# Kernel optimization log

Measured on AMD Instinct MI355X. Metric: run time of the kernel, lower is better.

The kernel has to match this reference:

```python
import jax, jax.numpy as jnp
import numpy as np
from jax import lax

S, B, D = 512, 64, 120          # seq_len, batch, input_dim
OC, K = 16, 6                   # conv out_channels, kernel_size
H, O = 1024, 48                 # lstm hidden, output_dim
AFTER_CONV = (D - K) + 1        # 115 (stride=1, pad=0, dil=1)
AFTER_POOL = AFTER_CONV - 1     # 114 (maxpool k=2, stride=1)
LSTM_IN = AFTER_POOL * OC       # 1824


def setup_inputs() -> dict:
    key = jax.random.key(0)
    ks = jax.random.split(key, 12)
    inp = {
        "input_": jax.random.normal(ks[0], (S, B, D), dtype=jnp.float32),
        "hidden": jnp.zeros((1, B, H), dtype=jnp.float32),
        "cell": jnp.zeros((1, B, H), dtype=jnp.float32),
        "conv_w": jax.random.normal(ks[1], (OC, 1, K), dtype=jnp.float32) * 0.1,
        "conv_b": jax.random.normal(ks[2], (OC,), dtype=jnp.float32) * 0.1,
        "w_ih": jax.random.normal(ks[3], (4 * H, LSTM_IN), dtype=jnp.float32) * 0.02,
        "w_hh": jax.random.normal(ks[4], (4 * H, H), dtype=jnp.float32) * 0.02,
        "b_ih": jax.random.normal(ks[5], (4 * H,), dtype=jnp.float32) * 0.02,
        "b_hh": jax.random.normal(ks[6], (4 * H,), dtype=jnp.float32) * 0.02,
        "h2h_w": jax.random.normal(ks[7], (H, H), dtype=jnp.float32) * 0.02,
        "h2h_b": jax.random.normal(ks[8], (H,), dtype=jnp.float32) * 0.02,
        "out_w": jax.random.normal(ks[9], (O, H), dtype=jnp.float32) * 0.02,
        "out_b": jax.random.normal(ks[10], (O,), dtype=jnp.float32) * 0.02,
    }
    return inp


def _forward(input_, hidden, cell, conv_w, conv_b, w_ih, w_hh, b_ih, b_hh,
             h2h_w, h2h_b, out_w, out_b):
    s, b, d = input_.shape
    # in_channels=1 -> context_len=0: per-step conv == batched conv over [S*B, 1, D]
    x = input_.reshape(s * b, 1, d)
    c = lax.conv_general_dilated(x, conv_w, window_strides=(1,), padding="VALID",
                                 dimension_numbers=("NCH", "OIH", "NCH"))
    c = jax.nn.relu(c + conv_b[None, :, None])            # [S*B, OC, AFTER_CONV]
    p = jnp.maximum(c[:, :, :-1], c[:, :, 1:])            # maxpool k=2 stride=1
    feat = p.reshape(s, b, -1)                            # [S, B, OC*AFTER_POOL]

    def step(carry, x_t):
        h, cst = carry
        gates = x_t @ w_ih.T + b_ih + h @ w_hh.T + b_hh   # [B, 4H]
        i, f, g, o = jnp.split(gates, 4, axis=-1)          # torch gate order i,f,g,o
        i = jax.nn.sigmoid(i); f = jax.nn.sigmoid(f)
        g = jnp.tanh(g); o = jax.nn.sigmoid(o)
        cst = f * cst + i * g
        h = o * jnp.tanh(cst)
        return (h, cst), h

    (_, _), hs = lax.scan(step, (hidden[0], cell[0]), feat)  # hs: [S, B, H]
    hs = jax.nn.relu(hs)
    h2 = jax.nn.relu(hs @ h2h_w.T + h2h_b)                # [S, B, H]
    logits = h2 @ out_w.T + out_b                         # [S, B, O]
    return jax.nn.log_softmax(logits, axis=-1)


def reference(input_, hidden, cell, conv_w, conv_b, w_ih, w_hh, b_ih, b_hh,
              h2h_w, h2h_b, out_w, out_b):
    return _forward(input_, hidden, cell, conv_w, conv_b, w_ih, w_hh, b_ih, b_hh,
                    h2h_w, h2h_b, out_w, out_b)
```

## Files before the change

### kernel.cpp

```cpp
#include <hip/hip_runtime.h>
#include <stdint.h>
#include <stddef.h>

#define kS 512
#define kB 64
#define kD 120
#define kOC 16
#define kKSZ 6
#define kPOOL 114
#define kLIN 1824
#define kLINP 1920
#define kH 1024
#define kG 4096
#define kO 48
#define kROWS (kS * kB)
#define RNB 256
#define SLOT 16384

typedef __attribute__((ext_vector_type(8))) short bf16x8;
typedef __attribute__((ext_vector_type(4))) float f32x4;

__device__ __forceinline__ unsigned short f32_to_bf16(float f) {
  unsigned u = __float_as_uint(f);
  u += 0x7FFFu + ((u >> 16) & 1u);
  return (unsigned short)(u >> 16);
}
__device__ __forceinline__ float bf16_to_f32(unsigned short h) {
  return __uint_as_float(((unsigned)h) << 16);
}
__device__ __forceinline__ float sigmoid_(float x) { return 1.f / (1.f + __expf(-x)); }
__device__ __forceinline__ float tanh_(float x) { return 1.f - 2.f / (__expf(2.f * x) + 1.f); }

__device__ __forceinline__ void load_lds_16(const void* g, void* l) {
  __builtin_amdgcn_global_load_lds((__attribute__((address_space(1))) void*)g,
                                   (__attribute__((address_space(3))) void*)l, 16, 0, 0);
}

__device__ __forceinline__ void bar_lgkm() {
  __builtin_amdgcn_sched_barrier(0);
  asm volatile("s_waitcnt lgkmcnt(0)" ::: "memory");
  __builtin_amdgcn_s_barrier();
  __builtin_amdgcn_sched_barrier(0);
}

__device__ __forceinline__ unsigned long long coh_load(const unsigned long long* p) {
  return __hip_atomic_load(p, __ATOMIC_RELAXED, __HIP_MEMORY_SCOPE_AGENT);
}
__device__ __forceinline__ void coh_store(unsigned long long* p, unsigned long long v) {
  __hip_atomic_store(p, v, __ATOMIC_RELAXED, __HIP_MEMORY_SCOPE_AGENT);
}
__device__ __forceinline__ int inval(unsigned long long q) {
  return ((q >> 7) & 0xFFull) == 0xFEull;
}

__global__ void convert_weights(const float* __restrict__ wih, const float* __restrict__ whh,
                                const float* __restrict__ h2hw, const float* __restrict__ outw,
                                const float* __restrict__ bih, const float* __restrict__ bhh,
                                unsigned short* __restrict__ wihb, unsigned short* __restrict__ whhb,
                                unsigned short* __restrict__ h2hwb, unsigned short* __restrict__ outwb,
                                float* __restrict__ bsum) {
  const size_t N0 = (size_t)kG * kLINP;
  const size_t N1 = (size_t)kG * kH;
  const size_t N2 = (size_t)kH * kH;
  const size_t N3 = (size_t)kO * kH;
  const size_t N4 = kG;
  const size_t TOT = N0 + N1 + N2 + N3 + N4;
  for (size_t i = (size_t)blockIdx.x * blockDim.x + threadIdx.x; i < TOT;
       i += (size_t)gridDim.x * blockDim.x) {
    if (i < N0) {
      const size_t row = i / kLINP;
      const int col = (int)(i % kLINP);
      wihb[i] = (col < kLIN) ? f32_to_bf16(wih[row * kLIN + col]) : 0;
    } else if (i < N0 + N1) whhb[i - N0] = f32_to_bf16(whh[i - N0]);
    else if (i < N0 + N1 + N2) h2hwb[i - N0 - N1] = f32_to_bf16(h2hw[i - N0 - N1]);
    else if (i < N0 + N1 + N2 + N3) outwb[i - N0 - N1 - N2] = f32_to_bf16(outw[i - N0 - N1 - N2]);
    else { size_t j = i - N0 - N1 - N2 - N3; bsum[j] = bih[j] + bhh[j]; }
  }
}

__global__ __launch_bounds__(256) void conv_pool(const float* __restrict__ x,
                                                 const float* __restrict__ cw,
                                                 const float* __restrict__ cb,
                                                 unsigned short* __restrict__ feat,
                                                 long row_base) {
  __shared__ float xs[8][kD];
  __shared__ float ws[kOC][kKSZ];
  __shared__ float bs[kOC];
  const int tid = threadIdx.x;
  const long grow0 = row_base + (long)blockIdx.x * 8;
  const long lrow0 = (long)blockIdx.x * 8;
  if (tid < kOC * kKSZ) ws[tid / kKSZ][tid % kKSZ] = cw[tid];
  if (tid < kOC) bs[tid] = cb[tid];
  for (int i = tid; i < 8 * kD; i += 256) xs[i / kD][i % kD] = x[grow0 * kD + i];
  __syncthreads();
  for (int r = 0; r < 8; ++r) {
    for (int idx = tid; idx < kLIN; idx += 256) {
      const int oc = idx / kPOOL, p = idx % kPOOL;
      float c0 = bs[oc], c1 = bs[oc];
#pragma unroll
      for (int k = 0; k < kKSZ; ++k) {
        c0 += xs[r][p + k] * ws[oc][k];
        c1 += xs[r][p + 1 + k] * ws[oc][k];
      }
      float v = fmaxf(fmaxf(c0, c1), 0.f);
      feat[(lrow0 + r) * kLINP + idx] = f32_to_bf16(v);
    }
    for (int idx = kLIN + tid; idx < kLINP; idx += 256)
      feat[(lrow0 + r) * kLINP + idx] = 0;
  }
}

__global__ __launch_bounds__(256) void gemm_bt_bf16(const unsigned short* __restrict__ A,
                                                    const unsigned short* __restrict__ B,
                                                    const float* __restrict__ bias,
                                                    unsigned short* __restrict__ C,
                                                    int N, int K) {
  __shared__ unsigned short Al[2][128 * 32];
  __shared__ unsigned short Bl[2][128 * 32];
  const int tid = threadIdx.x;
  const int lane = tid & 63;
  const int wid = tid >> 6;
  const int wm = wid >> 1, wn = wid & 1;
  const long bm = (long)blockIdx.x * 128;
  const long bn = (long)blockIdx.y * 128;
  const int NT = K / 32;

  f32x4 acc[4][4] = {};

  auto stage = [&](int buf, int kt) {
    const long k0 = (long)kt * 32;
#pragma unroll
    for (int rnd = 0; rnd < 2; ++rnd) {
      const int chunk = rnd * 256 + tid;
      const int r = chunk >> 2, c = chunk & 3;
      load_lds_16(A + (bm + r) * K + k0 + c * 8, &Al[buf][chunk * 8]);
      load_lds_16(B + (bn + r) * K + k0 + c * 8, &Bl[buf][chunk * 8]);
    }
  };

  stage(0, 0);
  __syncthreads();
  int buf = 0;
  for (int kt = 0; kt < NT; ++kt) {
    if (kt + 1 < NT) stage(buf ^ 1, kt + 1);
    bf16x8 af[4], bfr[4];
#pragma unroll
    for (int i = 0; i < 4; ++i) {
      const int ar = wm * 64 + i * 16 + (lane & 15);
      af[i] = *(const bf16x8*)&Al[buf][ar * 32 + (lane >> 4) * 8];
      const int bc = wn * 64 + i * 16 + (lane & 15);
      bfr[i] = *(const bf16x8*)&Bl[buf][bc * 32 + (lane >> 4) * 8];
    }
#pragma unroll
    for (int i = 0; i < 4; ++i)
#pragma unroll
      for (int j = 0; j < 4; ++j)
        acc[i][j] = __builtin_amdgcn_mfma_f32_16x16x32_bf16(af[i], bfr[j], acc[i][j], 0, 0, 0);
    __syncthreads();
    buf ^= 1;
  }

#pragma unroll
  for (int i = 0; i < 4; ++i) {
#pragma unroll
    for (int j = 0; j < 4; ++j) {
      const long col = bn + wn * 64 + j * 16 + (lane & 15);
      const float bv = bias[col];
#pragma unroll
      for (int e = 0; e < 4; ++e) {
        const long row = bm + wm * 64 + i * 16 + (lane >> 4) * 4 + e;
        C[row * N + col] = f32_to_bf16(fmaxf(acc[i][j][e] + bv, 0.f));
      }
    }
  }
}

__global__ __launch_bounds__(512, 2) void gemm256_m2(const unsigned short* __restrict__ A,
                                                     const unsigned short* __restrict__ B,
                                                     const float* __restrict__ bias,
                                                     unsigned short* __restrict__ C,
                                                     int Kp) {
  __shared__ unsigned short AL[2][2][128 * 64];
  __shared__ unsigned short BL[2][2][128 * 64];
  const int tid = threadIdx.x;
  const int lane = tid & 63;
  const int wid = tid >> 6;
  const int wm = wid >> 2;
  const int wn = wid & 3;
  const long bm = (long)blockIdx.x * 256;
  const long bn = (long)blockIdx.y * 256;
  const int iters = Kp / 128;
  const int nkt = iters * 2;

  f32x4 acc[8][4] = {};

  auto stageu = [&](int db, int op, int hf, int kt) {
    const unsigned short* S = op ? B : A;
    const long base = op ? bn : bm;
    unsigned short* L = op ? &BL[db][hf][0] : &AL[db][hf][0];
#pragma unroll
    for (int c = 0; c < 2; ++c) {
      const int ch = c * 512 + tid;
      const int r = ch >> 3;
      const int cb = (ch & 7) * 8;
      load_lds_16(S + (base + hf * 128 + r) * Kp + (long)kt * 64 + cb, L + r * 64 + cb);
    }
  };

#pragma unroll
  for (int kt = 0; kt < 2; ++kt)
#pragma unroll
    for (int u = 0; u < 4; ++u) stageu(0, u >> 1, u & 1, kt);
  __builtin_amdgcn_sched_barrier(0);
  asm volatile("s_waitcnt vmcnt(0)" ::: "memory");
  __builtin_amdgcn_s_barrier();
  __builtin_amdgcn_sched_barrier(0);

  int d = 0;
  for (int it = 0; it < iters; ++it, d ^= 1) {
    bf16x8 bfr[8];
#pragma unroll
    for (int p = 0; p < 8; ++p) {
      const int q = p & 3;
      const int kbase = (p >> 2) ? 1 : 0;
      if (q == 0) {
#pragma unroll
        for (int nf = 0; nf < 4; ++nf)
#pragma unroll
          for (int ks = 0; ks < 2; ++ks)
            bfr[nf * 2 + ks] = *(const bf16x8*)&BL[d][wn >> 1]
                [((wn & 1) * 64 + nf * 16 + (lane & 15)) * 64 + ks * 32 + (lane >> 4) * 8];
      }
      bf16x8 afr[2][2];
#pragma unroll
      for (int m2 = 0; m2 < 2; ++m2)
#pragma unroll
        for (int ks = 0; ks < 2; ++ks)
          afr[m2][ks] = *(const bf16x8*)&AL[d][wm]
              [((q * 2 + m2) * 16 + (lane & 15)) * 64 + ks * 32 + (lane >> 4) * 8];
      (void)kbase;
      const int ktN = it * 2 + 2 + (p >> 2);
      if (ktN < nkt) stageu(d ^ 1, q >> 1, q & 1, ktN);
      if (p == 3 || p == 7) {
        __builtin_amdgcn_sched_barrier(0);
        asm volatile("s_waitcnt vmcnt(8)" ::: "memory");
      }
      __builtin_amdgcn_s_barrier();
      __builtin_amdgcn_s_setprio(1);
#pragma unroll
      for (int m2 = 0; m2 < 2; ++m2)
#pragma unroll
        for (int nf = 0; nf < 4; ++nf)
#pragma unroll
          for (int ks = 0; ks < 2; ++ks)
            acc[q * 2 + m2][nf] = __builtin_amdgcn_mfma_f32_16x16x32_bf16(
                afr[m2][ks], bfr[nf * 2 + ks], acc[q * 2 + m2][nf], 0, 0, 0);
      __builtin_amdgcn_s_setprio(0);
      __builtin_amdgcn_s_barrier();
    }
  }


#pragma unroll
  for (int mf = 0; mf < 8; ++mf) {
#pragma unroll
    for (int nf = 0; nf < 4; ++nf) {
      const long col = bn + wn * 64 + nf * 16 + (lane & 15);
      const float bv = bias[col];
      const int g = (int)(col >> 10), ub = (int)((col >> 4) & 63), ur = (int)(col & 15);
#pragma unroll
      for (int e = 0; e < 4; ++e) {
        const long row = bm + wm * 128 + mf * 16 + (lane >> 4) * 4 + e;
        C[(row * 64 + ub) * 64 + g * 16 + ur] = f32_to_bf16(acc[mf][nf][e] + bv);
      }
    }
  }
}

__global__ __launch_bounds__(512) void lstm_rec(const unsigned short* __restrict__ xw,
                                                const unsigned short* __restrict__ whh,
                                                const float* __restrict__ h0,
                                                const float* __restrict__ c0,
                                                float* __restrict__ cst,
                                                unsigned long long* __restrict__ hbuf,
                                                unsigned short* __restrict__ hs,
                                                int nsteps, int first, int t0step) {
  __shared__ unsigned short Bl[64 * 1024];
  __shared__ unsigned short hstage[256];
  __shared__ unsigned pacc_h[8][2][4][64];
  const int tid = threadIdx.x;
  const int lane = tid & 63;
  const int kq = tid >> 6;
  const int urow = lane & 15;
  const int bq = lane >> 4;
  const int bid = blockIdx.x;
  const int ublk = bid & 63;
  const int bqtr = bid >> 6;
  const int u0 = ublk * 16;
  const bool gatewave = (kq < 4);
  const int gbL = bq * 4 + kq;
  const int gbW = bqtr * 16 + gbL;

  for (int idx = tid; idx < 64 * 128; idx += 512) {
    const int col = idx & 63;
    const int kc = idx >> 6;
    const int gcol = (col >> 4) * kH + u0 + (col & 15);
    *(bf16x8*)&Bl[kc * 512 + col * 8] = *(const bf16x8*)&whh[(long)gcol * kH + kc * 8];
  }
  float creg = 0.f;
  if (first) {
    if (tid < 64) {
      const int lb = tid >> 2, un4 = (tid & 3) * 4, gb = bqtr * 16 + lb;
      unsigned long long v = 0;
#pragma unroll
      for (int e = 0; e < 4; ++e) {
        const unsigned long long b16 = f32_to_bf16(h0[gb * kH + u0 + un4 + e]);
        v |= b16 << (16 * e);
      }
      coh_store(&hbuf[(size_t)ublk * 256 + gb * 4 + (tid & 3)], v);
    }
    if (gatewave) creg = c0[gbW * kH + u0 + urow];
  } else {
    if (gatewave) creg = cst[gbW * kH + u0 + urow];
  }
  bar_lgkm();

  float xv[4];
  auto load_xv = [&](int t) {
    const unsigned short* xp = xw + ((long)(t * kB + gbW) * 64 + ublk) * 64 + urow;
#pragma unroll
    for (int g = 0; g < 4; ++g) xv[g] = bf16_to_f32(xp[g * 16]);
  };
  if (gatewave) load_xv(0);

  const int ach = (bqtr * 16 + urow) * 4 + (bq & 1) * 2;

  for (int t = 0; t < nsteps; ++t) {
    const unsigned long long* curs = hbuf + (size_t)(t0step + t) * SLOT;
    unsigned long long* nxts = hbuf + (size_t)(t0step + t + 1) * SLOT;

    unsigned long long q[8];
#pragma unroll
    for (int i = 0; i < 8; ++i)
      q[i] = coh_load(curs + (size_t)((kq * 4 + (i >> 1)) * 2 + (bq >> 1)) * 256 + ach + (i & 1));
    for (;;) {
      int bad = 0;
#pragma unroll
      for (int i = 0; i < 8; ++i) bad |= inval(q[i]);
      if (!bad) break;
      unsigned long long t2[8];
#pragma unroll
      for (int i = 0; i < 8; ++i)
        t2[i] =
            coh_load(curs + (size_t)((kq * 4 + (i >> 1)) * 2 + (bq >> 1)) * 256 + ach + (i & 1));
#pragma unroll
      for (int i = 0; i < 8; ++i) q[i] = t2[i];
    }

    f32x4 acc[4] = {};
#pragma unroll
    for (int ktl = 0; ktl < 4; ++ktl) {
      union { unsigned long long qq[2]; bf16x8 v; } a;
      a.qq[0] = q[2 * ktl];
      a.qq[1] = q[2 * ktl + 1];
      const int kc = (kq * 4 + ktl) * 4 + bq;
#pragma unroll
      for (int g = 0; g < 4; ++g) {
        const bf16x8 bb = *(const bf16x8*)&Bl[kc * 512 + (g * 16 + urow) * 8];
        acc[g] = __builtin_amdgcn_mfma_f32_16x16x32_bf16(a.v, bb, acc[g], 0, 0, 0);
      }
    }

#pragma unroll
    for (int j = 0; j < 4; ++j)
#pragma unroll
      for (int gp = 0; gp < 2; ++gp) {
        const unsigned lo = f32_to_bf16(acc[2 * gp][j]);
        const unsigned hi = f32_to_bf16(acc[2 * gp + 1][j]);
        pacc_h[kq][gp][j][lane] = lo | (hi << 16);
      }
    bar_lgkm();

    if (gatewave) {
      float s[4] = {xv[0], xv[1], xv[2], xv[3]};
#pragma unroll
      for (int p = 0; p < 8; ++p) {
        const unsigned v0 = pacc_h[p][0][kq][lane];
        const unsigned v1 = pacc_h[p][1][kq][lane];
        s[0] += bf16_to_f32((unsigned short)v0);
        s[1] += bf16_to_f32((unsigned short)(v0 >> 16));
        s[2] += bf16_to_f32((unsigned short)v1);
        s[3] += bf16_to_f32((unsigned short)(v1 >> 16));
      }
      const float gi = sigmoid_(s[0]);
      const float gf = sigmoid_(s[1]);
      const float gg = tanh_(s[2]);
      const float go = sigmoid_(s[3]);
      creg = gf * creg + gi * gg;
      hstage[gbL * 16 + urow] = f32_to_bf16(go * tanh_(creg));
      asm volatile("" ::: "memory");
      if (lane < 16) {
        const int lb = (lane >> 2) * 4 + kq;
        const int e = lane & 3;
        unsigned long long qp = 0;
#pragma unroll
        for (int x = 0; x < 4; ++x)
          qp |= ((unsigned long long)hstage[lb * 16 + e * 4 + x]) << (16 * x);
        coh_store(&nxts[(size_t)ublk * 256 + (bqtr * 16 + lb) * 4 + e], qp);
        unsigned long long r = 0;
#pragma unroll
        for (int x = 0; x < 4; ++x) {
          unsigned long long sv = (qp >> (16 * x)) & 0xFFFFull;
          if (sv & 0x8000ull) sv = 0;
          r |= sv << (16 * x);
        }
        *(unsigned long long*)&hs[(long)(t * kB + bqtr * 16 + lb) * kH + u0 + e * 4] = r;
      }
      if (t + 1 < nsteps) load_xv(t + 1);
    }
    bar_lgkm();
  }

  if (gatewave) cst[gbW * kH + u0 + urow] = creg;
}

__global__ __launch_bounds__(256) void out_head(const unsigned short* __restrict__ h2,
                                                const unsigned short* __restrict__ ow,
                                                const float* __restrict__ ob,
                                                float* __restrict__ out) {
  __shared__ unsigned short Wl[48 * 1024];
  const int tid = threadIdx.x;
  const int lane = tid & 63;
  const int w = tid >> 6;
  for (int idx = tid; idx < 48 * 128; idx += 256) {
    const int col = idx % 48;
    const int kc = idx / 48;
    *(bf16x8*)&Wl[kc * 384 + col * 8] = *(const bf16x8*)&ow[(long)col * kH + kc * 8];
  }
  __syncthreads();
  const long row0 = (long)blockIdx.x * 64 + w * 16;
  f32x4 acc[3] = {};
  const unsigned short* arow = h2 + (row0 + (lane & 15)) * kH + (lane >> 4) * 8;
#pragma unroll 8
  for (int kt = 0; kt < 32; ++kt) {
    const bf16x8 a = *(const bf16x8*)(arow + kt * 32);
    const int kc = kt * 4 + (lane >> 4);
#pragma unroll
    for (int n = 0; n < 3; ++n) {
      const bf16x8 bb = *(const bf16x8*)&Wl[kc * 384 + (n * 16 + (lane & 15)) * 8];
      acc[n] = __builtin_amdgcn_mfma_f32_16x16x32_bf16(a, bb, acc[n], 0, 0, 0);
    }
  }
  const int colb = lane & 15;
#pragma unroll
  for (int j = 0; j < 4; ++j) {
    float v[3];
#pragma unroll
    for (int n = 0; n < 3; ++n) v[n] = acc[n][j] + ob[n * 16 + colb];
    float m = fmaxf(fmaxf(v[0], v[1]), v[2]);
#pragma unroll
    for (int s = 1; s < 16; s <<= 1) m = fmaxf(m, __shfl_xor(m, s, 64));
    float se = __expf(v[0] - m) + __expf(v[1] - m) + __expf(v[2] - m);
#pragma unroll
    for (int s = 1; s < 16; s <<= 1) se += __shfl_xor(se, s, 64);
    const float lse = m + __logf(se);
    const long row = row0 + (lane >> 4) * 4 + j;
#pragma unroll
    for (int n = 0; n < 3; ++n) out[row * 48 + n * 16 + colb] = v[n] - lse;
  }
}

extern "C" void kernel_launch(void* const* d_in, const int* in_sizes, int n_in,
                              void* d_out, int out_size, void* d_ws, size_t ws_size,
                              hipStream_t stream) {
  const float* input_ = (const float*)d_in[0];
  const float* hidden = (const float*)d_in[1];
  const float* cell = (const float*)d_in[2];
  const float* conv_w = (const float*)d_in[3];
  const float* conv_b = (const float*)d_in[4];
  const float* w_ih = (const float*)d_in[5];
  const float* w_hh = (const float*)d_in[6];
  const float* b_ih = (const float*)d_in[7];
  const float* b_hh = (const float*)d_in[8];
  const float* h2h_w = (const float*)d_in[9];
  const float* h2h_b = (const float*)d_in[10];
  const float* out_w = (const float*)d_in[11];
  const float* out_b = (const float*)d_in[12];
  float* out = (float*)d_out;

  const size_t HBUF_BYTES = (size_t)(kS + 1) * SLOT * 8;

  const size_t FIXED = ((size_t)kG * kLINP + (size_t)kG * kH + (size_t)kH * kH +
                        (size_t)kO * kH) * 2 +
                       (size_t)kG * 4 +
                       HBUF_BYTES +
                       (size_t)kB * kH * 4 +
                       16 * 256;

  int CHUNK = 4;
  const int cand[] = {512, 256, 128, 64, 32, 16, 8, 4};
  for (int i = 0; i < 8; ++i) {
    const size_t rowsC = (size_t)cand[i] * kB;
    const size_t need = FIXED + rowsC * (kLINP + kG) * 2;
    if (need <= ws_size) { CHUNK = cand[i]; break; }
  }
  const size_t rowsC = (size_t)CHUNK * kB;

  char* ws = (char*)d_ws;
  size_t off = 0;
  auto alloc = [&](size_t bytes) {
    char* p = ws + off;
    off += (bytes + 255) & ~(size_t)255;
    return p;
  };
  unsigned short* regionA = (unsigned short*)alloc(rowsC * kLINP * 2);
  unsigned short* regionB = (unsigned short*)alloc(rowsC * kG * 2);
  unsigned short* wih_b = (unsigned short*)alloc((size_t)kG * kLINP * 2);
  unsigned short* whh_b = (unsigned short*)alloc((size_t)kG * kH * 2);
  unsigned short* h2hw_b = (unsigned short*)alloc((size_t)kH * kH * 2);
  unsigned short* outw_b = (unsigned short*)alloc((size_t)kO * kH * 2);
  float* bias_sum = (float*)alloc((size_t)kG * 4);
  unsigned long long* hbuf = (unsigned long long*)alloc(HBUF_BYTES);
  float* cstate = (float*)alloc((size_t)kB * kH * 4);

  unsigned short* feat_c = regionA;
  unsigned short* hs_c = regionA;
  unsigned short* xw_c = regionB;
  unsigned short* h2_c = regionB;

  hipMemsetAsync(hbuf, 0x7F, HBUF_BYTES, stream);
  convert_weights<<<2048, 256, 0, stream>>>(w_ih, w_hh, h2h_w, out_w, b_ih, b_hh, wih_b, whh_b,
                                            h2hw_b, outw_b, bias_sum);

  const int nch = kS / CHUNK;
  for (int ci = 0; ci < nch; ++ci) {
    const long t0 = (long)ci * CHUNK;
    conv_pool<<<(int)(rowsC / 8), 256, 0, stream>>>(input_, conv_w, conv_b, feat_c, t0 * kB);
    gemm256_m2<<<dim3((int)(rowsC / 256), kG / 256), 512, 0, stream>>>(feat_c, wih_b, bias_sum,
                                                                       xw_c, kLINP);
    lstm_rec<<<RNB, 512, 0, stream>>>(xw_c, whh_b, hidden, cell, cstate, hbuf, hs_c, CHUNK,
                                      ci == 0 ? 1 : 0, (int)t0);
    gemm_bt_bf16<<<dim3((int)(rowsC / 128), kH / 128), 256, 0, stream>>>(hs_c, h2hw_b, h2h_b,
                                                                         h2_c, kH, kH);
    out_head<<<(int)(rowsC / 64), 256, 0, stream>>>(h2_c, outw_b, out_b, out + t0 * kB * kO);
  }
}
```

Before: 2.017 ms.

## Rework input-projection GEMM to 256x128 tiles with triple-buffered k-major LDS

```diff
diff --git a/kernel.cpp b/kernel.cpp
--- a/kernel.cpp
+++ b/kernel.cpp
@@ -175,97 +175,108 @@
   }
 }
 
-__global__ __launch_bounds__(512, 2) void gemm256_m2(const unsigned short* __restrict__ A,
-                                                     const unsigned short* __restrict__ B,
-                                                     const float* __restrict__ bias,
-                                                     unsigned short* __restrict__ C,
-                                                     int Kp) {
-  __shared__ unsigned short AL[2][2][128 * 64];
-  __shared__ unsigned short BL[2][2][128 * 64];
+__global__ __launch_bounds__(512) void gemm256_m2(const unsigned short* __restrict__ A,
+                                                  const unsigned short* __restrict__ B,
+                                                  const float* __restrict__ bias,
+                                                  unsigned short* __restrict__ C, int Kp) {
+  __shared__ unsigned short ALb[3][2048 * 8];
+  __shared__ unsigned short BLb[3][1024 * 8];
   const int tid = threadIdx.x;
   const int lane = tid & 63;
   const int wid = tid >> 6;
   const int wm = wid >> 2;
   const int wn = wid & 3;
   const long bm = (long)blockIdx.x * 256;
-  const long bn = (long)blockIdx.y * 256;
-  const int iters = Kp / 128;
-  const int nkt = iters * 2;
-
-  f32x4 acc[8][4] = {};
-
-  auto stageu = [&](int db, int op, int hf, int kt) {
-    const unsigned short* S = op ? B : A;
-    const long base = op ? bn : bm;
-    unsigned short* L = op ? &BL[db][hf][0] : &AL[db][hf][0];
-#pragma unroll
-    for (int c = 0; c < 2; ++c) {
-      const int ch = c * 512 + tid;
-      const int r = ch >> 3;
-      const int cb = (ch & 7) * 8;
-      load_lds_16(S + (base + hf * 128 + r) * Kp + (long)kt * 64 + cb, L + r * 64 + cb);
+  const long bn = (long)blockIdx.y * 128;
+  const int nkt = Kp / 64;
+
+  f32x4 acc[8][2] = {};
+
+  auto stage_unit = [&](int buf, int u, int kt) {
+    if (u < 2) {
+#pragma unroll
+      for (int c = 0; c < 2; ++c) {
+        const int L = u * 1024 + c * 512 + tid;
+        const int kc = L >> 8, row = L & 255;
+        load_lds_16(A + (bm + row) * Kp + (long)kt * 64 + kc * 8, &ALb[buf][L * 8]);
+      }
+    } else {
+#pragma unroll
+      for (int c = 0; c < 2; ++c) {
+        const int L = c * 512 + tid;
+        const int kc = L >> 7, row = L & 127;
+        load_lds_16(B + (bn + row) * Kp + (long)kt * 64 + kc * 8, &BLb[buf][L * 8]);
+      }
     }
   };
 
 #pragma unroll
-  for (int kt = 0; kt < 2; ++kt)
-#pragma unroll
-    for (int u = 0; u < 4; ++u) stageu(0, u >> 1, u & 1, kt);
+  for (int u = 0; u < 3; ++u) stage_unit(0, u, 0);
+#pragma unroll
+  for (int u = 0; u < 3; ++u) stage_unit(1, u, 1);
   __builtin_amdgcn_sched_barrier(0);
-  asm volatile("s_waitcnt vmcnt(0)" ::: "memory");
+  asm volatile("s_waitcnt vmcnt(6)" ::: "memory");
   __builtin_amdgcn_s_barrier();
   __builtin_amdgcn_sched_barrier(0);
 
-  int d = 0;
-  for (int it = 0; it < iters; ++it, d ^= 1) {
-    bf16x8 bfr[8];
-#pragma unroll
-    for (int p = 0; p < 8; ++p) {
-      const int q = p & 3;
-      const int kbase = (p >> 2) ? 1 : 0;
-      if (q == 0) {
-#pragma unroll
-        for (int nf = 0; nf < 4; ++nf)
-#pragma unroll
-          for (int ks = 0; ks < 2; ++ks)
-            bfr[nf * 2 + ks] = *(const bf16x8*)&BL[d][wn >> 1]
-                [((wn & 1) * 64 + nf * 16 + (lane & 15)) * 64 + ks * 32 + (lane >> 4) * 8];
-      }
+  int buf = 0;
+  for (int kt = 0; kt < nkt; ++kt) {
+    int nbuf = buf + 2;
+    if (nbuf >= 3) nbuf -= 3;
+
+    bf16x8 bfr[2][2];
+#pragma unroll
+    for (int nf = 0; nf < 2; ++nf)
+#pragma unroll
+      for (int ks = 0; ks < 2; ++ks) {
+        const int row = wn * 32 + nf * 16 + (lane & 15);
+        const int kc = ks * 4 + (lane >> 4);
+        bfr[nf][ks] = *(const bf16x8*)&BLb[buf][(kc * 128 + row) * 8];
+      }
+
+#pragma unroll
+    for (int q = 0; q < 4; ++q) {
       bf16x8 afr[2][2];
 #pragma unroll
       for (int m2 = 0; m2 < 2; ++m2)
 #pragma unroll
-        for (int ks = 0; ks < 2; ++ks)
-          afr[m2][ks] = *(const bf16x8*)&AL[d][wm]
-              [((q * 2 + m2) * 16 + (lane & 15)) * 64 + ks * 32 + (lane >> 4) * 8];
-      (void)kbase;
-      const int ktN = it * 2 + 2 + (p >> 2);
-      if (ktN < nkt) stageu(d ^ 1, q >> 1, q & 1, ktN);
-      if (p == 3 || p == 7) {
-        __builtin_amdgcn_sched_barrier(0);
-        asm volatile("s_waitcnt vmcnt(8)" ::: "memory");
-      }
-      __builtin_amdgcn_s_barrier();
+        for (int ks = 0; ks < 2; ++ks) {
+          const int row = wm * 128 + (q * 2 + m2) * 16 + (lane & 15);
+          const int kc = ks * 4 + (lane >> 4);
+          afr[m2][ks] = *(const bf16x8*)&ALb[buf][(kc * 256 + row) * 8];
+        }
+      if (q < 3 && kt + 2 < nkt) stage_unit(nbuf, q, kt + 2);
       __builtin_amdgcn_s_setprio(1);
 #pragma unroll
       for (int m2 = 0; m2 < 2; ++m2)
 #pragma unroll
-        for (int nf = 0; nf < 4; ++nf)
+        for (int nf = 0; nf < 2; ++nf)
 #pragma unroll
           for (int ks = 0; ks < 2; ++ks)
             acc[q * 2 + m2][nf] = __builtin_amdgcn_mfma_f32_16x16x32_bf16(
-                afr[m2][ks], bfr[nf * 2 + ks], acc[q * 2 + m2][nf], 0, 0, 0);
+                afr[m2][ks], bfr[nf][ks], acc[q * 2 + m2][nf], 0, 0, 0);
       __builtin_amdgcn_s_setprio(0);
+    }
+
+    if (kt < nkt - 1) {
+      __builtin_amdgcn_sched_barrier(0);
+      if (kt + 2 < nkt) {
+        asm volatile("s_waitcnt vmcnt(6)" ::: "memory");
+      } else {
+        asm volatile("s_waitcnt vmcnt(0)" ::: "memory");
+      }
       __builtin_amdgcn_s_barrier();
-    }
-  }
-
+      __builtin_amdgcn_sched_barrier(0);
+    }
+    buf = buf + 1;
+    if (buf >= 3) buf = 0;
+  }
 
 #pragma unroll
   for (int mf = 0; mf < 8; ++mf) {
 #pragma unroll
-    for (int nf = 0; nf < 4; ++nf) {
-      const long col = bn + wn * 64 + nf * 16 + (lane & 15);
+    for (int nf = 0; nf < 2; ++nf) {
+      const long col = bn + wn * 32 + nf * 16 + (lane & 15);
       const float bv = bias[col];
       const int g = (int)(col >> 10), ub = (int)((col >> 4) & 63), ur = (int)(col & 15);
 #pragma unroll
@@ -536,7 +547,7 @@
   for (int ci = 0; ci < nch; ++ci) {
     const long t0 = (long)ci * CHUNK;
     conv_pool<<<(int)(rowsC / 8), 256, 0, stream>>>(input_, conv_w, conv_b, feat_c, t0 * kB);
-    gemm256_m2<<<dim3((int)(rowsC / 256), kG / 256), 512, 0, stream>>>(feat_c, wih_b, bias_sum,
+    gemm256_m2<<<dim3((int)(rowsC / 256), kG / 128), 512, 0, stream>>>(feat_c, wih_b, bias_sum,
                                                                        xw_c, kLINP);
     lstm_rec<<<RNB, 512, 0, stream>>>(xw_c, whh_b, hidden, cell, cstate, hbuf, hs_c, CHUNK,
                                       ci == 0 ? 1 : 0, (int)t0);
```

New measurement: 2.281 ms. 13.1% more time.
